# Kernel optimization log

Measured on AMD Instinct MI355X. Metric: run time of the kernel, lower is better.

Reference implementation:

```python
import jax, jax.numpy as jnp
import numpy as np

N_EMBED = 1024
HEAD_SIZE = 128
B, T = 4, 4096

def setup_inputs() -> dict:
    key = jax.random.key(0)
    kx, kk, kq, kv = jax.random.split(key, 4)
    s = (1.0 / np.sqrt(N_EMBED)).astype(np.float32)
    return {
        "x": jax.random.normal(kx, (B, T, N_EMBED), dtype=jnp.float32),
        "W_key": jax.random.normal(kk, (N_EMBED, HEAD_SIZE), dtype=jnp.float32) * s,
        "W_query": jax.random.normal(kq, (N_EMBED, HEAD_SIZE), dtype=jnp.float32) * s,
        "W_value": jax.random.normal(kv, (N_EMBED, HEAD_SIZE), dtype=jnp.float32) * s,
    }

def reference(x, W_key, W_query, W_value):
    # x: [B,T,C]; single-head causal attention. NOTE: scale is C**-0.5 (n_embed),
    # matching the original source (not head_size**-0.5).
    Bn, Tn, C = x.shape
    k = jnp.einsum('btc,cd->btd', x, W_key)    # [B,T,d]
    q = jnp.einsum('btc,cd->btd', x, W_query)  # [B,T,d]
    v = jnp.einsum('btc,cd->btd', x, W_value)  # [B,T,d]
    scores = jnp.einsum('btd,bsd->bts', q, k) * (C ** -0.5)  # [B,T,T]
    causal = jnp.tril(jnp.ones((Tn, Tn), dtype=bool))
    scores = jnp.where(causal[None, :, :], scores, -jnp.inf)
    attn = jax.nn.softmax(scores, axis=-1)
    return jnp.einsum('bts,bsd->btd', attn, v)
```

## Files before the change

kernel.cpp:

```cpp
#include <hip/hip_runtime.h>
#include <hip/hip_bf16.h>

typedef __attribute__((ext_vector_type(8))) short bf16x8;
typedef __attribute__((ext_vector_type(4))) float f32x4;
typedef __attribute__((ext_vector_type(4))) unsigned short us4;

__device__ __forceinline__ unsigned short f2bf(float f) {
    union { float f; unsigned u; } c; c.f = f;
    unsigned u = c.u;
    u += 0x7fffu + ((u >> 16) & 1u);
    return (unsigned short)(u >> 16);
}
__device__ __forceinline__ float bf2f(unsigned short h) {
    union { unsigned u; float f; } c; c.u = ((unsigned)h) << 16;
    return c.f;
}

#define QSCALE 0.04508422f

__global__ __launch_bounds__(256) void wconv_kernel(
        const float* __restrict__ Wk, const float* __restrict__ Wq,
        const float* __restrict__ Wv, unsigned short* __restrict__ WbT) {
    int idx = blockIdx.x * 256 + threadIdx.x;
    int n = idx >> 10, kk = idx & 1023;
    const float* W = (n < 128) ? Wk : (n < 256) ? Wq : Wv;
    int col = n & 127;
    WbT[idx] = f2bf(W[kk * 128 + col]);
}

__global__ __launch_bounds__(512) void qkv_gemm_kernel(
        const float* __restrict__ x, const unsigned short* __restrict__ WbT,
        unsigned short* __restrict__ kw, unsigned short* __restrict__ qw,
        unsigned short* __restrict__ vTw) {
    __shared__ __align__(16) unsigned short Al[64 * 72];
    __shared__ __align__(16) unsigned short Bl[384 * 72];
    const int tid = threadIdx.x;
    const int m0 = blockIdx.x * 64;
    const int w = tid >> 6, l = tid & 63;
    const int l15 = l & 15, lh = l >> 4;

    f32x4 acc[4][3] = {};

    const int ar = tid >> 3, ac = (tid & 7) * 8;

    float4 aV0, aV1;
    bf16x8 bV[6];

    auto issue = [&](int k0) {
        const float* src = &x[(size_t)(m0 + ar) * 1024 + k0 + ac];
        aV0 = *(const float4*)src;
        aV1 = *(const float4*)(src + 4);
        for (int it = 0; it < 6; ++it) {
            int idx = it * 512 + tid;
            bV[it] = *(const bf16x8*)&WbT[(size_t)(idx >> 3) * 1024 + k0 + (idx & 7) * 8];
        }
    };

    issue(0);
    for (int t = 0; t < 16; ++t) {
        {
            union { unsigned short u[8]; bf16x8 v; } pk;
            pk.u[0] = f2bf(aV0.x); pk.u[1] = f2bf(aV0.y);
            pk.u[2] = f2bf(aV0.z); pk.u[3] = f2bf(aV0.w);
            pk.u[4] = f2bf(aV1.x); pk.u[5] = f2bf(aV1.y);
            pk.u[6] = f2bf(aV1.z); pk.u[7] = f2bf(aV1.w);
            *(bf16x8*)&Al[ar * 72 + ac] = pk.v;
        }
        for (int it = 0; it < 6; ++it) {
            int idx = it * 512 + tid;
            *(bf16x8*)&Bl[(idx >> 3) * 72 + (idx & 7) * 8] = bV[it];
        }
        __syncthreads();
        if (t + 1 < 16) issue((t + 1) * 64);
        for (int kc = 0; kc < 2; ++kc) {
            bf16x8 a[4], bb[3];
            for (int mi = 0; mi < 4; ++mi)
                a[mi] = *(bf16x8*)&Al[(mi * 16 + l15) * 72 + kc * 32 + lh * 8];
            for (int ni = 0; ni < 3; ++ni)
                bb[ni] = *(bf16x8*)&Bl[(w * 48 + ni * 16 + l15) * 72 + kc * 32 + lh * 8];
            for (int mi = 0; mi < 4; ++mi)
                for (int ni = 0; ni < 3; ++ni)
                    acc[mi][ni] = __builtin_amdgcn_mfma_f32_16x16x32_bf16(
                            a[mi], bb[ni], acc[mi][ni], 0, 0, 0);
        }
        __syncthreads();
    }

    for (int mi = 0; mi < 4; ++mi)
        for (int ni = 0; ni < 3; ++ni) {
            int col = w * 48 + ni * 16 + l15;
            int sect = col >> 7, cc = col & 127;
            if (sect < 2) {
                unsigned short* dst = (sect == 0) ? kw : qw;
                float fs = (sect == 0) ? 1.0f : QSCALE;
                for (int i = 0; i < 4; ++i) {
                    int row = m0 + mi * 16 + lh * 4 + i;
                    dst[(size_t)row * 128 + cc] = f2bf(acc[mi][ni][i] * fs);
                }
            } else {
                int trow0 = m0 + mi * 16 + lh * 4;
                int b = trow0 >> 12, t0 = trow0 & 4095;
                union { unsigned short u[4]; us4 v; } pk;
                for (int i = 0; i < 4; ++i) pk.u[i] = f2bf(acc[mi][ni][i]);
                *(us4*)&vTw[((size_t)(b * 128 + cc)) * 4096 + t0] = pk.v;
            }
        }
}

__global__ __launch_bounds__(512) void attn_kernel(
        const unsigned short* __restrict__ kw, const unsigned short* __restrict__ qw,
        const unsigned short* __restrict__ vTw,
        unsigned short* __restrict__ pO, float* __restrict__ pL,
        int nCPB, int G, int TPC) {
    __shared__ __align__(16) unsigned short Kl[64 * 128];
    __shared__ __align__(16) unsigned short Vl[128 * 64];
    __shared__ __align__(16) unsigned short Pl[8][1024];

    const int tid = threadIdx.x;
    const int wgid = blockIdx.x;
    const int xcd = wgid & 7, slot = wgid >> 3;
    const int b = xcd >> 1, half = xcd & 1;
    const int cid = (nCPB - 1) - (slot * 2 + half);
    const int halfG = G >> 1;
    int a = 0;
    while (halfG * (a + 1) * (a + 2) <= cid) ++a;
    int rem = cid - halfG * a * (a + 1);
    const int g = G * a + rem / (a + 1);
    const int c = rem % (a + 1);
    const int kt0 = c * TPC;
    const int kt1 = min(kt0 + TPC, 2 * g + 2);

    const int w = tid >> 6, l = tid & 63;
    const int l15 = l & 15, lh = l >> 4;
    const int qrow0 = g * 128 + w * 16;

    bf16x8 qa[4];
    {
        size_t grow = (size_t)b * 4096 + qrow0 + l15;
        for (int cc = 0; cc < 4; ++cc)
            qa[cc] = *(const bf16x8*)&qw[grow * 128 + cc * 32 + lh * 8];
    }
    bf16x8 ones;
    for (int u = 0; u < 8; ++u) ones[u] = (short)0x3F80;

    f32x4 o[8] = {};
    f32x4 lsa = {0.f, 0.f, 0.f, 0.f};

    const int kr_ = tid >> 3;
    const int vd_ = tid >> 2;
    bf16x8 kReg[2], vReg[2];
    auto issue = [&](int kt) {
        int kv0 = kt * 64;
        const unsigned short* ks = &kw[((size_t)(b * 4096 + kv0 + kr_)) * 128 + (tid & 7) * 16];
        kReg[0] = *(const bf16x8*)ks;
        kReg[1] = *(const bf16x8*)(ks + 8);
        const unsigned short* vs = &vTw[((size_t)(b * 128 + vd_)) * 4096 + kv0 + (tid & 3) * 16];
        vReg[0] = *(const bf16x8*)vs;
        vReg[1] = *(const bf16x8*)(vs + 8);
    };

    char* Plw = (char*)&Pl[w][0];

    issue(kt0);
    for (int kt = kt0; kt < kt1; ++kt) {
        __syncthreads();
        for (int it = 0; it < 2; ++it)
            *(bf16x8*)((char*)Kl + kr_ * 256 +
                    (((tid & 7) * 32 + it * 16) ^ ((kr_ & 7) << 4))) = kReg[it];
        for (int it = 0; it < 2; ++it)
            *(bf16x8*)((char*)Vl + vd_ * 128 +
                    (((tid & 3) * 32 + it * 16) ^ ((vd_ & 7) << 4))) = vReg[it];
        __syncthreads();
        if (kt + 1 < kt1) issue(kt + 1);

        const int kv0 = kt * 64;
        if (kv0 > qrow0 + 15) continue;

        f32x4 s[4];
        __builtin_amdgcn_s_setprio(1);
        for (int ni = 0; ni < 4; ++ni) {
            s[ni] = (f32x4){0.f, 0.f, 0.f, 0.f};
            int kr = ni * 16 + l15;
            int sw = (kr & 7) << 4;
            for (int cc = 0; cc < 4; ++cc) {
                bf16x8 bk = *(bf16x8*)((char*)Kl + kr * 256 + ((lh * 16 + cc * 64) ^ sw));
                s[ni] = __builtin_amdgcn_mfma_f32_16x16x32_bf16(qa[cc], bk, s[ni], 0, 0, 0);
            }
        }
        __builtin_amdgcn_s_setprio(0);

        if (kv0 + 63 > qrow0) {
            for (int ni = 0; ni < 4; ++ni)
                for (int i = 0; i < 4; ++i)
                    if (kv0 + ni * 16 + l15 > qrow0 + lh * 4 + i) s[ni][i] = -INFINITY;
        }
        for (int ni = 0; ni < 4; ++ni)
            for (int i = 0; i < 4; ++i) {
                float p = exp2f(s[ni][i]);
                int q = lh * 4 + i;
                *(unsigned short*)(Plw + q * 128 +
                        ((ni * 32 + l15 * 2) ^ ((q & 7) << 4))) = f2bf(p);
            }
        bf16x8 pa[2];
        for (int kc = 0; kc < 2; ++kc)
            pa[kc] = *(bf16x8*)(Plw + l15 * 128 +
                    ((kc * 64 + lh * 16) ^ ((l15 & 7) << 4)));
        __builtin_amdgcn_s_setprio(1);
        lsa = __builtin_amdgcn_mfma_f32_16x16x32_bf16(pa[1], ones,
              __builtin_amdgcn_mfma_f32_16x16x32_bf16(pa[0], ones, lsa, 0, 0, 0), 0, 0, 0);
        for (int nd = 0; nd < 8; ++nd) {
            int dr = nd * 16 + l15;
            int sw = (dr & 7) << 4;
            for (int kc = 0; kc < 2; ++kc) {
                bf16x8 bv = *(bf16x8*)((char*)Vl + dr * 128 + ((lh * 16 + kc * 64) ^ sw));
                o[nd] = __builtin_amdgcn_mfma_f32_16x16x32_bf16(pa[kc], bv, o[nd], 0, 0, 0);
            }
        }
        __builtin_amdgcn_s_setprio(0);
    }

    const int slot_ = b * nCPB + cid;
    unsigned short* po = pO + (size_t)slot_ * 16384;
    for (int nd = 0; nd < 8; ++nd)
        for (int i = 0; i < 4; ++i)
            po[(w * 16 + lh * 4 + i) * 128 + nd * 16 + l15] = f2bf(o[nd][i]);
    if (l15 == 0) {
        float* pl = pL + (size_t)slot_ * 128;
        for (int i = 0; i < 4; ++i)
            pl[w * 16 + lh * 4 + i] = lsa[i];
    }
}

__global__ __launch_bounds__(256) void combine_kernel(
        const unsigned short* __restrict__ pO, const float* __restrict__ pL,
        float* __restrict__ out, int nCPB, int G) {
    int idx = blockIdx.x * 256 + threadIdx.x;
    int row = idx >> 4, d8 = (idx & 15) * 8;
    int b = row >> 12, t = row & 4095;
    int g = t >> 7, rowin = t & 127;
    int a = g / G;
    int nch = a + 1;
    int base = b * nCPB + (G >> 1) * a * (a + 1) + (g - G * a) * (a + 1);

    float den = 0.f;
    float num[8] = {0.f, 0.f, 0.f, 0.f, 0.f, 0.f, 0.f, 0.f};
    for (int cc = 0; cc < nch; ++cc) {
        den += pL[(size_t)(base + cc) * 128 + rowin];
        bf16x8 ov = *(const bf16x8*)&pO[(size_t)(base + cc) * 16384 + rowin * 128 + d8];
        for (int u = 0; u < 8; ++u)
            num[u] += bf2f((unsigned short)ov[u]);
    }
    float inv = 1.f / den;
    for (int u = 0; u < 8; ++u)
        out[(size_t)row * 128 + d8 + u] = num[u] * inv;
}

extern "C" void kernel_launch(void* const* d_in, const int* in_sizes, int n_in,
                              void* d_out, int out_size, void* d_ws, size_t ws_size,
                              hipStream_t stream) {
    const float* x  = (const float*)d_in[0];
    const float* Wk = (const float*)d_in[1];
    const float* Wq = (const float*)d_in[2];
    const float* Wv = (const float*)d_in[3];
    float* out = (float*)d_out;

    char* ws = (char*)d_ws;
    unsigned short* WbT = (unsigned short*)(ws);
    unsigned short* kw  = (unsigned short*)(ws + 786432);
    unsigned short* qw  = (unsigned short*)(ws + 786432 + 4194304);
    unsigned short* vTw = (unsigned short*)(ws + 786432 + 2 * 4194304);
    size_t base = 786432 + 3 * (size_t)4194304;

    int nCPB, G, TPC;
    size_t need4 = base + (size_t)1088 * 32768 + (size_t)1088 * 512;
    if (ws_size >= need4) { nCPB = 272; G = 2; TPC = 4; }
    else                  { nCPB = 144; G = 4; TPC = 8; }
    int nslots = 4 * nCPB;
    unsigned short* pO = (unsigned short*)(ws + base);
    float*          pL = (float*)(ws + base + (size_t)nslots * 32768);

    wconv_kernel<<<1536, 256, 0, stream>>>(Wk, Wq, Wv, WbT);
    qkv_gemm_kernel<<<256, 512, 0, stream>>>(x, WbT, kw, qw, vTw);
    attn_kernel<<<nslots, 512, 0, stream>>>(kw, qw, vTw, pO, pL, nCPB, G, TPC);
    combine_kernel<<<1024, 256, 0, stream>>>(pO, pL, out, nCPB, G);
}
```

Measured before the change: 93.54 us.

## Halve QKV GEMM row tile, transpose score MFMA, use packed bf16 conversion

The QKV projection GEMM now uses 32-row tiles with 512 blocks instead of 64-row tiles with 256, so more workgroups are spread across CUs. Each wave now computes a 16x96 output tile rather than 64x48. In attention, the QK^T MFMA swaps its operands so each lane holds scores for one query across four consecutive keys. That lets P be packed with v_cvt_pk_bf16_f32 and written to LDS as 8-byte stores instead of scalar 2-byte stores. The trade-off is less reuse of weight tiles per block in the GEMM and twice as many B-tile loads overall.

```diff
diff --git a/kernel.cpp b/kernel.cpp
--- a/kernel.cpp
+++ b/kernel.cpp
@@ -14,6 +14,11 @@
 __device__ __forceinline__ float bf2f(unsigned short h) {
     union { unsigned u; float f; } c; c.u = ((unsigned)h) << 16;
     return c.f;
+}
+__device__ __forceinline__ unsigned cvt_pk_bf16(float lo, float hi) {
+    unsigned r;
+    asm volatile("v_cvt_pk_bf16_f32 %0, %1, %2" : "=v"(r) : "v"(lo), "v"(hi));
+    return r;
 }
 
 #define QSCALE 0.04508422f
@@ -32,24 +37,23 @@
         const float* __restrict__ x, const unsigned short* __restrict__ WbT,
         unsigned short* __restrict__ kw, unsigned short* __restrict__ qw,
         unsigned short* __restrict__ vTw) {
-    __shared__ __align__(16) unsigned short Al[64 * 72];
+    __shared__ __align__(16) unsigned short Al[32 * 72];
     __shared__ __align__(16) unsigned short Bl[384 * 72];
     const int tid = threadIdx.x;
-    const int m0 = blockIdx.x * 64;
+    const int m0 = blockIdx.x * 32;
     const int w = tid >> 6, l = tid & 63;
     const int l15 = l & 15, lh = l >> 4;
-
-    f32x4 acc[4][3] = {};
-
-    const int ar = tid >> 3, ac = (tid & 7) * 8;
-
-    float4 aV0, aV1;
+    const int wr = w >> 2, wc = w & 3;
+
+    f32x4 acc[6] = {};
+
+    const int ar = tid >> 4, ac = (tid & 15) * 4;
+
+    float4 aV;
     bf16x8 bV[6];
 
     auto issue = [&](int k0) {
-        const float* src = &x[(size_t)(m0 + ar) * 1024 + k0 + ac];
-        aV0 = *(const float4*)src;
-        aV1 = *(const float4*)(src + 4);
+        aV = *(const float4*)&x[(size_t)(m0 + ar) * 1024 + k0 + ac];
         for (int it = 0; it < 6; ++it) {
             int idx = it * 512 + tid;
             bV[it] = *(const bf16x8*)&WbT[(size_t)(idx >> 3) * 1024 + k0 + (idx & 7) * 8];
@@ -59,12 +63,10 @@
     issue(0);
     for (int t = 0; t < 16; ++t) {
         {
-            union { unsigned short u[8]; bf16x8 v; } pk;
-            pk.u[0] = f2bf(aV0.x); pk.u[1] = f2bf(aV0.y);
-            pk.u[2] = f2bf(aV0.z); pk.u[3] = f2bf(aV0.w);
-            pk.u[4] = f2bf(aV1.x); pk.u[5] = f2bf(aV1.y);
-            pk.u[6] = f2bf(aV1.z); pk.u[7] = f2bf(aV1.w);
-            *(bf16x8*)&Al[ar * 72 + ac] = pk.v;
+            uint2 p;
+            p.x = cvt_pk_bf16(aV.x, aV.y);
+            p.y = cvt_pk_bf16(aV.z, aV.w);
+            *(uint2*)&Al[ar * 72 + ac] = p;
         }
         for (int it = 0; it < 6; ++it) {
             int idx = it * 512 + tid;
@@ -73,38 +75,33 @@
         __syncthreads();
         if (t + 1 < 16) issue((t + 1) * 64);
         for (int kc = 0; kc < 2; ++kc) {
-            bf16x8 a[4], bb[3];
-            for (int mi = 0; mi < 4; ++mi)
-                a[mi] = *(bf16x8*)&Al[(mi * 16 + l15) * 72 + kc * 32 + lh * 8];
-            for (int ni = 0; ni < 3; ++ni)
-                bb[ni] = *(bf16x8*)&Bl[(w * 48 + ni * 16 + l15) * 72 + kc * 32 + lh * 8];
-            for (int mi = 0; mi < 4; ++mi)
-                for (int ni = 0; ni < 3; ++ni)
-                    acc[mi][ni] = __builtin_amdgcn_mfma_f32_16x16x32_bf16(
-                            a[mi], bb[ni], acc[mi][ni], 0, 0, 0);
-        }
-        __syncthreads();
-    }
-
-    for (int mi = 0; mi < 4; ++mi)
-        for (int ni = 0; ni < 3; ++ni) {
-            int col = w * 48 + ni * 16 + l15;
-            int sect = col >> 7, cc = col & 127;
-            if (sect < 2) {
-                unsigned short* dst = (sect == 0) ? kw : qw;
-                float fs = (sect == 0) ? 1.0f : QSCALE;
-                for (int i = 0; i < 4; ++i) {
-                    int row = m0 + mi * 16 + lh * 4 + i;
-                    dst[(size_t)row * 128 + cc] = f2bf(acc[mi][ni][i] * fs);
-                }
-            } else {
-                int trow0 = m0 + mi * 16 + lh * 4;
-                int b = trow0 >> 12, t0 = trow0 & 4095;
-                union { unsigned short u[4]; us4 v; } pk;
-                for (int i = 0; i < 4; ++i) pk.u[i] = f2bf(acc[mi][ni][i]);
-                *(us4*)&vTw[((size_t)(b * 128 + cc)) * 4096 + t0] = pk.v;
-            }
-        }
+            bf16x8 a = *(bf16x8*)&Al[(wr * 16 + l15) * 72 + kc * 32 + lh * 8];
+            for (int ni = 0; ni < 6; ++ni) {
+                bf16x8 bb = *(bf16x8*)&Bl[(wc * 96 + ni * 16 + l15) * 72 + kc * 32 + lh * 8];
+                acc[ni] = __builtin_amdgcn_mfma_f32_16x16x32_bf16(a, bb, acc[ni], 0, 0, 0);
+            }
+        }
+        __syncthreads();
+    }
+
+    for (int ni = 0; ni < 6; ++ni) {
+        int col = wc * 96 + ni * 16 + l15;
+        int sect = col >> 7, cc = col & 127;
+        if (sect < 2) {
+            unsigned short* dst = (sect == 0) ? kw : qw;
+            float fs = (sect == 0) ? 1.0f : QSCALE;
+            for (int i = 0; i < 4; ++i) {
+                int row = m0 + wr * 16 + lh * 4 + i;
+                dst[(size_t)row * 128 + cc] = f2bf(acc[ni][i] * fs);
+            }
+        } else {
+            int trow0 = m0 + wr * 16 + lh * 4;
+            int b = trow0 >> 12, t0 = trow0 & 4095;
+            union { unsigned short u[4]; us4 v; } pk;
+            for (int i = 0; i < 4; ++i) pk.u[i] = f2bf(acc[ni][i]);
+            *(us4*)&vTw[((size_t)(b * 128 + cc)) * 4096 + t0] = pk.v;
+        }
+    }
 }
 
 __global__ __launch_bounds__(512) void attn_kernel(
@@ -184,23 +181,25 @@
             int sw = (kr & 7) << 4;
             for (int cc = 0; cc < 4; ++cc) {
                 bf16x8 bk = *(bf16x8*)((char*)Kl + kr * 256 + ((lh * 16 + cc * 64) ^ sw));
-                s[ni] = __builtin_amdgcn_mfma_f32_16x16x32_bf16(qa[cc], bk, s[ni], 0, 0, 0);
+                s[ni] = __builtin_amdgcn_mfma_f32_16x16x32_bf16(bk, qa[cc], s[ni], 0, 0, 0);
             }
         }
         __builtin_amdgcn_s_setprio(0);
 
         if (kv0 + 63 > qrow0) {
+            int qg = qrow0 + l15;
             for (int ni = 0; ni < 4; ++ni)
                 for (int i = 0; i < 4; ++i)
-                    if (kv0 + ni * 16 + l15 > qrow0 + lh * 4 + i) s[ni][i] = -INFINITY;
-        }
-        for (int ni = 0; ni < 4; ++ni)
-            for (int i = 0; i < 4; ++i) {
-                float p = exp2f(s[ni][i]);
-                int q = lh * 4 + i;
-                *(unsigned short*)(Plw + q * 128 +
-                        ((ni * 32 + l15 * 2) ^ ((q & 7) << 4))) = f2bf(p);
-            }
+                    if (kv0 + ni * 16 + lh * 4 + i > qg) s[ni][i] = -INFINITY;
+        }
+        for (int ni = 0; ni < 4; ++ni) {
+            float p0 = exp2f(s[ni][0]), p1 = exp2f(s[ni][1]);
+            float p2 = exp2f(s[ni][2]), p3 = exp2f(s[ni][3]);
+            uint2 pk;
+            pk.x = cvt_pk_bf16(p0, p1);
+            pk.y = cvt_pk_bf16(p2, p3);
+            *(uint2*)(Plw + l15 * 128 + ((ni * 32 + lh * 8) ^ ((l15 & 7) << 4))) = pk;
+        }
         bf16x8 pa[2];
         for (int kc = 0; kc < 2; ++kc)
             pa[kc] = *(bf16x8*)(Plw + l15 * 128 +
@@ -280,7 +279,7 @@
     float*          pL = (float*)(ws + base + (size_t)nslots * 32768);
 
     wconv_kernel<<<1536, 256, 0, stream>>>(Wk, Wq, Wv, WbT);
-    qkv_gemm_kernel<<<256, 512, 0, stream>>>(x, WbT, kw, qw, vTw);
+    qkv_gemm_kernel<<<512, 512, 0, stream>>>(x, WbT, kw, qw, vTw);
     attn_kernel<<<nslots, 512, 0, stream>>>(kw, qw, vTw, pO, pL, nCPB, G, TPC);
     combine_kernel<<<1024, 256, 0, stream>>>(pO, pL, out, nCPB, G);
 }
```

After: 85.24 us. 8.9% less time.
